# Performance work log

Hardware: AMD Instinct MI355X
Metric: run time of the kernel (lower is better)

Reference implementation:

```python
import jax, jax.numpy as jnp
import numpy as np

EMBED_DIM = 768
NUM_HEADS = 12
HEAD_DIM = EMBED_DIM // NUM_HEADS


def setup_inputs() -> dict:
    key = jax.random.key(0)
    k1, k2, k3 = jax.random.split(key, 3)
    B, T = 128, 128
    x = jax.random.normal(k1, (B, T, EMBED_DIM), dtype=jnp.float32)
    # weights stored as [in, out] so forward is x @ W (equivalent to torch Linear, bias=False)
    w_qkv = jax.random.normal(k2, (EMBED_DIM, 3 * EMBED_DIM), dtype=jnp.float32) * (EMBED_DIM ** -0.5)
    w_proj = jax.random.normal(k3, (EMBED_DIM, EMBED_DIM), dtype=jnp.float32) * (EMBED_DIM ** -0.5)
    return {"x": x, "w_qkv": w_qkv, "w_proj": w_proj}


def reference(x, w_qkv, w_proj):
    B, T, C = x.shape
    # fused QKV projection -> (3, B, H, T, D)
    qkv = (x @ w_qkv).reshape(B, T, 3, NUM_HEADS, HEAD_DIM)
    q, k, v = jnp.transpose(qkv, (2, 0, 3, 1, 4))
    # scaled dot-product scores (B, H, T, T)
    att = jnp.einsum('bhqd,bhkd->bhqk', q, k) * (HEAD_DIM ** -0.5)
    causal = jnp.tril(jnp.ones((T, T), dtype=bool))
    att = jnp.where(causal, att, -jnp.inf)
    # float32 softmax then cast back (matches att.float().softmax().to(x.dtype))
    att = jax.nn.softmax(att.astype(jnp.float32), axis=-1).astype(x.dtype)
    # dropout is identity in eval/reference mode
    out = jnp.einsum('bhqk,bhkd->bhqd', att, v)          # (B, H, T, D)
    out = jnp.transpose(out, (0, 2, 1, 3)).reshape(B, T, C)
    return out @ w_proj
```

## Files before the change

kernel.cpp:

```cpp
#include <hip/hip_runtime.h>

typedef __bf16 bf16_t;
typedef bf16_t bf16x8 __attribute__((ext_vector_type(8)));
typedef bf16_t bf16x4 __attribute__((ext_vector_type(4)));
typedef float f32x4 __attribute__((ext_vector_type(4)));

__device__ __forceinline__ f32x4 mfma16(bf16x8 a, bf16x8 b, f32x4 c) {
  return __builtin_amdgcn_mfma_f32_16x16x32_bf16(a, b, c, 0, 0, 0);
}

__device__ __forceinline__ void gload16(const bf16_t* g, bf16_t* l) {
  __builtin_amdgcn_global_load_lds(
      (const __attribute__((address_space(1))) void*)g,
      (__attribute__((address_space(3))) void*)l, 16, 0, 0);
}

__global__ void convert_kernel(const float* __restrict__ in, bf16_t* __restrict__ out, int n4) {
  int i = blockIdx.x * blockDim.x + threadIdx.x;
  if (i < n4) {
    float4 v = ((const float4*)in)[i];
    bf16x4 o;
    o[0] = (bf16_t)v.x; o[1] = (bf16_t)v.y; o[2] = (bf16_t)v.z; o[3] = (bf16_t)v.w;
    *(bf16x4*)&out[(size_t)i * 4] = o;
  }
}

__global__ void transpose_conv_kernel(const float* __restrict__ in, bf16_t* __restrict__ out,
                                      int K, int N) {
  __shared__ bf16_t tile[32][33];
  const int n0 = blockIdx.x * 32, k0 = blockIdx.y * 32;
  const int tx = threadIdx.x & 31, ty = threadIdx.x >> 5;
#pragma unroll
  for (int ph = 0; ph < 4; ++ph) {
    int k = ty + ph * 8;
    tile[k][tx] = (bf16_t)in[(size_t)(k0 + k) * N + n0 + tx];
  }
  __syncthreads();
#pragma unroll
  for (int ph = 0; ph < 4; ++ph) {
    int n = ty + ph * 8;
    out[(size_t)(n0 + n) * K + k0 + tx] = tile[tx][n];
  }
}

template <bool F32OUT>
__global__ __launch_bounds__(256, 2) void gemm_kernel(
    const bf16_t* __restrict__ A, const bf16_t* __restrict__ Bt,
    void* __restrict__ Cout, int M, int N, int K) {
  __shared__ bf16_t As[2][128 * 64];
  __shared__ bf16_t Bs[2][128 * 64];
  const int tid = threadIdx.x;
  const int lane = tid & 63;
  const int w = tid >> 6;
  const int wm = w >> 1, wn = w & 1;
  const int lr = lane & 15, kg = lane >> 4;
  const int bm = blockIdx.y, bn = blockIdx.x;
  const bf16_t* Ab = A + (size_t)bm * 128 * K;
  const bf16_t* Bb = Bt + (size_t)bn * 128 * K;

  f32x4 acc[4][4];
#pragma unroll
  for (int i = 0; i < 4; ++i)
#pragma unroll
    for (int j = 0; j < 4; ++j) acc[i][j] = (f32x4){0.f, 0.f, 0.f, 0.f};

  const int NKT = K >> 6;
  const int sr = tid >> 3;
  const int sslot = tid & 7;

  auto stage = [&](int buf, int kt) {
    const int k0 = kt << 6;
#pragma unroll
    for (int it = 0; it < 4; ++it) {
      int r = it * 32 + sr;
      int kofs = (sslot ^ (r & 7)) << 3;
      int lidx = (it * 256 + tid) << 3;
      gload16(Ab + (size_t)r * K + (k0 + kofs), &As[buf][lidx]);
      gload16(Bb + (size_t)r * K + (k0 + kofs), &Bs[buf][lidx]);
    }
  };

  stage(0, 0);
  __syncthreads();

  for (int kt = 0; kt < NKT; ++kt) {
    const int buf = kt & 1;
    if (kt + 1 < NKT) stage(buf ^ 1, kt + 1);
#pragma unroll
    for (int kk = 0; kk < 2; ++kk) {
      const int slot = ((kk << 2) + kg) ^ (lr & 7);
      bf16x8 af[4], bfv[4];
#pragma unroll
      for (int mt = 0; mt < 4; ++mt) {
        int r = wm * 64 + mt * 16 + lr;
        af[mt] = *(const bf16x8*)&As[buf][(r << 6) + (slot << 3)];
      }
#pragma unroll
      for (int nt = 0; nt < 4; ++nt) {
        int r = wn * 64 + nt * 16 + lr;
        bfv[nt] = *(const bf16x8*)&Bs[buf][(r << 6) + (slot << 3)];
      }
#pragma unroll
      for (int mt = 0; mt < 4; ++mt)
#pragma unroll
        for (int nt = 0; nt < 4; ++nt)
          acc[mt][nt] = mfma16(af[mt], bfv[nt], acc[mt][nt]);
    }
    __syncthreads();
  }

  const int row0 = bm * 128 + wm * 64 + kg * 4;
  const int col0 = bn * 128 + wn * 64 + lr;
#pragma unroll
  for (int mt = 0; mt < 4; ++mt)
#pragma unroll
    for (int nt = 0; nt < 4; ++nt)
#pragma unroll
      for (int rr = 0; rr < 4; ++rr) {
        size_t idx = (size_t)(row0 + mt * 16 + rr) * N + (col0 + nt * 16);
        if constexpr (F32OUT)
          ((float*)Cout)[idx] = acc[mt][nt][rr];
        else
          ((bf16_t*)Cout)[idx] = (bf16_t)acc[mt][nt][rr];
      }
}

#define ATT_H 12
__global__ __launch_bounds__(256, 2) void attn_kernel(const bf16_t* __restrict__ qkv,
                                                      bf16_t* __restrict__ obuf) {
  __shared__ bf16_t Ks[128 * 72];
  __shared__ bf16_t Vt[64 * 136];
  __shared__ bf16_t Ps[128 * 136];
  const int tid = threadIdx.x, lane = tid & 63, w = tid >> 6;
  const int lr = lane & 15, kg = lane >> 4;
  const int bh = blockIdx.x;
  const int b = bh / ATT_H, h = bh % ATT_H;
  const size_t base = (size_t)b * 128 * 2304;
  const int hoff = h * 64;

#pragma unroll
  for (int it = 0; it < 4; ++it) {
    int idx = it * 256 + tid;
    int r = idx >> 3, slot = idx & 7;
    bf16x8 v = *(const bf16x8*)&qkv[base + (size_t)r * 2304 + 768 + hoff + slot * 8];
    *(bf16x8*)&Ks[r * 72 + slot * 8] = v;
  }
#pragma unroll 4
  for (int it = 0; it < 32; ++it) {
    int idx = it * 256 + tid;
    int t = idx >> 6, d = idx & 63;
    Vt[d * 136 + t] = qkv[base + (size_t)t * 2304 + 1536 + hoff + d];
  }
  const int qrow0 = w * 32;
  bf16x8 qf[2][2];
#pragma unroll
  for (int mt = 0; mt < 2; ++mt)
#pragma unroll
    for (int kk = 0; kk < 2; ++kk)
      qf[mt][kk] = *(const bf16x8*)&qkv[base + (size_t)(qrow0 + mt * 16 + lr) * 2304 + hoff +
                                        kk * 32 + kg * 8];
  __syncthreads();

  const int NT = 2 * w + 2;
  f32x4 acc[2][8];
#pragma unroll
  for (int mt = 0; mt < 2; ++mt)
#pragma unroll
    for (int nt = 0; nt < 8; ++nt) acc[mt][nt] = (f32x4){0.f, 0.f, 0.f, 0.f};

#pragma unroll
  for (int nt = 0; nt < 8; ++nt) {
    if (nt < NT) {
#pragma unroll
      for (int kk = 0; kk < 2; ++kk) {
        bf16x8 kf = *(const bf16x8*)&Ks[(nt * 16 + lr) * 72 + kk * 32 + kg * 8];
        acc[0][nt] = mfma16(qf[0][kk], kf, acc[0][nt]);
        acc[1][nt] = mfma16(qf[1][kk], kf, acc[1][nt]);
      }
    }
  }

#pragma unroll
  for (int mt = 0; mt < 2; ++mt) {
#pragma unroll
    for (int rr = 0; rr < 4; ++rr) {
      const int row = qrow0 + mt * 16 + kg * 4 + rr;
      float m = -1e30f;
#pragma unroll
      for (int nt = 0; nt < 8; ++nt) {
        if (nt < NT) {
          int col = nt * 16 + lr;
          float s = acc[mt][nt][rr] * 0.125f;
          s = (col <= row) ? s : -1e30f;
          acc[mt][nt][rr] = s;
          m = fmaxf(m, s);
        }
      }
      m = fmaxf(m, __shfl_xor(m, 1));
      m = fmaxf(m, __shfl_xor(m, 2));
      m = fmaxf(m, __shfl_xor(m, 4));
      m = fmaxf(m, __shfl_xor(m, 8));
      float ssum = 0.f;
#pragma unroll
      for (int nt = 0; nt < 8; ++nt) {
        if (nt < NT) {
          float p = __builtin_amdgcn_exp2f((acc[mt][nt][rr] - m) * 1.44269504f);
          acc[mt][nt][rr] = p;
          ssum += p;
        }
      }
      ssum += __shfl_xor(ssum, 1);
      ssum += __shfl_xor(ssum, 2);
      ssum += __shfl_xor(ssum, 4);
      ssum += __shfl_xor(ssum, 8);
      float inv = 1.0f / ssum;
#pragma unroll
      for (int nt = 0; nt < 8; ++nt) {
        if (nt < NT) Ps[row * 136 + nt * 16 + lr] = (bf16_t)(acc[mt][nt][rr] * inv);
      }
    }
  }

  f32x4 oacc[2][4];
#pragma unroll
  for (int mt = 0; mt < 2; ++mt)
#pragma unroll
    for (int dt = 0; dt < 4; ++dt) oacc[mt][dt] = (f32x4){0.f, 0.f, 0.f, 0.f};

  const int KS = w + 1;
#pragma unroll
  for (int ks = 0; ks < 4; ++ks) {
    if (ks < KS) {
      bf16x8 pa0 = *(const bf16x8*)&Ps[(qrow0 + lr) * 136 + ks * 32 + kg * 8];
      bf16x8 pa1 = *(const bf16x8*)&Ps[(qrow0 + 16 + lr) * 136 + ks * 32 + kg * 8];
#pragma unroll
      for (int dt = 0; dt < 4; ++dt) {
        bf16x8 vb = *(const bf16x8*)&Vt[(dt * 16 + lr) * 136 + ks * 32 + kg * 8];
        oacc[0][dt] = mfma16(pa0, vb, oacc[0][dt]);
        oacc[1][dt] = mfma16(pa1, vb, oacc[1][dt]);
      }
    }
  }

#pragma unroll
  for (int mt = 0; mt < 2; ++mt)
#pragma unroll
    for (int dt = 0; dt < 4; ++dt)
#pragma unroll
      for (int rr = 0; rr < 4; ++rr) {
        int t = qrow0 + mt * 16 + kg * 4 + rr;
        obuf[((size_t)b * 128 + t) * 768 + hoff + dt * 16 + lr] = (bf16_t)oacc[mt][dt][rr];
      }
}

extern "C" void kernel_launch(void* const* d_in, const int* in_sizes, int n_in,
                              void* d_out, int out_size, void* d_ws, size_t ws_size,
                              hipStream_t stream) {
  const float* x = (const float*)d_in[0];
  const float* w_qkv = (const float*)d_in[1];
  const float* w_proj = (const float*)d_in[2];
  float* out = (float*)d_out;
  char* ws = (char*)d_ws;

  bf16_t* xb     = (bf16_t*)(ws);
  bf16_t* wqkvt  = (bf16_t*)(ws + 25165824);
  bf16_t* wprojt = (bf16_t*)(ws + 28704768);
  bf16_t* qkv    = (bf16_t*)(ws + 29884416);
  bf16_t* obuf   = (bf16_t*)(ws + 105381888);

  convert_kernel<<<dim3(12288), dim3(256), 0, stream>>>(x, xb, 3145728);
  transpose_conv_kernel<<<dim3(72, 24), dim3(256), 0, stream>>>(w_qkv, wqkvt, 768, 2304);
  transpose_conv_kernel<<<dim3(24, 24), dim3(256), 0, stream>>>(w_proj, wprojt, 768, 768);
  gemm_kernel<false><<<dim3(18, 128), dim3(256), 0, stream>>>(xb, wqkvt, (void*)qkv, 16384, 2304, 768);
  attn_kernel<<<dim3(1536), dim3(256), 0, stream>>>(qkv, obuf);
  gemm_kernel<true><<<dim3(6, 128), dim3(256), 0, stream>>>(obuf, wprojt, (void*)out, 16384, 768, 768);
}
```

Baseline: 172.2 us.

## Replace GEMM with 256x256 8-wave pipelined kernel and XCD-aware block swizzle

Both projection GEMMs now use a new 512-thread kernel computing 256x256 output tiles, where each wave owns a 128x64 sub-tile. Global-to-LDS loads for later k-tiles are interleaved between MFMA quads under explicit vmcnt waits and barriers, and MFMA priority is raised with setprio. The 1D grid is remapped so consecutive tiles land on the same XCD for better L2 reuse. This aims to hide load latency and cut LDS traffic per FLOP. In exchange it uses 128KB of LDS per block, adds many barriers, and leaves fewer blocks for the small output projection (192 blocks).

```diff
diff --git a/kernel.cpp b/kernel.cpp
--- a/kernel.cpp
+++ b/kernel.cpp
@@ -14,6 +14,14 @@
       (const __attribute__((address_space(1))) void*)g,
       (__attribute__((address_space(3))) void*)l, 16, 0, 0);
 }
+
+#define BARRIER()                      \
+  do {                                 \
+    asm volatile("" ::: "memory");     \
+    __builtin_amdgcn_s_barrier();      \
+    asm volatile("" ::: "memory");     \
+  } while (0)
+#define VMCNT(n) asm volatile("s_waitcnt vmcnt(" #n ")" ::: "memory")
 
 __global__ void convert_kernel(const float* __restrict__ in, bf16_t* __restrict__ out, int n4) {
   int i = blockIdx.x * blockDim.x + threadIdx.x;
@@ -44,75 +52,148 @@
 }
 
 template <bool F32OUT>
-__global__ __launch_bounds__(256, 2) void gemm_kernel(
+__global__ __launch_bounds__(512, 2) void gemm8_kernel(
     const bf16_t* __restrict__ A, const bf16_t* __restrict__ Bt,
-    void* __restrict__ Cout, int M, int N, int K) {
-  __shared__ bf16_t As[2][128 * 64];
-  __shared__ bf16_t Bs[2][128 * 64];
+    void* __restrict__ Cout, int M, int N, int K, int nbn) {
+  __shared__ bf16_t As[2][256 * 64];
+  __shared__ bf16_t Bs[2][256 * 64];
   const int tid = threadIdx.x;
   const int lane = tid & 63;
   const int w = tid >> 6;
-  const int wm = w >> 1, wn = w & 1;
+  const int wm = w >> 2, wn = w & 3;
   const int lr = lane & 15, kg = lane >> 4;
-  const int bm = blockIdx.y, bn = blockIdx.x;
-  const bf16_t* Ab = A + (size_t)bm * 128 * K;
-  const bf16_t* Bb = Bt + (size_t)bn * 128 * K;
-
-  f32x4 acc[4][4];
-#pragma unroll
-  for (int i = 0; i < 4; ++i)
+
+  const int nwg = gridDim.x;
+  const int cpx = nwg >> 3;
+  const int bid = blockIdx.x;
+  const int sid = (bid & 7) * cpx + (bid >> 3);
+  const int bm = sid / nbn, bn = sid % nbn;
+
+  const bf16_t* Ab = A + (size_t)bm * 256 * K;
+  const bf16_t* Bb = Bt + (size_t)bn * 256 * K;
+
+  f32x4 acc[8][4];
+#pragma unroll
+  for (int i = 0; i < 8; ++i)
 #pragma unroll
     for (int j = 0; j < 4; ++j) acc[i][j] = (f32x4){0.f, 0.f, 0.f, 0.f};
 
   const int NKT = K >> 6;
-  const int sr = tid >> 3;
-  const int sslot = tid & 7;
-
-  auto stage = [&](int buf, int kt) {
-    const int k0 = kt << 6;
-#pragma unroll
-    for (int it = 0; it < 4; ++it) {
-      int r = it * 32 + sr;
-      int kofs = (sslot ^ (r & 7)) << 3;
-      int lidx = (it * 256 + tid) << 3;
-      gload16(Ab + (size_t)r * K + (k0 + kofs), &As[buf][lidx]);
-      gload16(Bb + (size_t)r * K + (k0 + kofs), &Bs[buf][lidx]);
-    }
-  };
-
-  stage(0, 0);
-  __syncthreads();
-
-  for (int kt = 0; kt < NKT; ++kt) {
-    const int buf = kt & 1;
-    if (kt + 1 < NKT) stage(buf ^ 1, kt + 1);
-#pragma unroll
-    for (int kk = 0; kk < 2; ++kk) {
-      const int slot = ((kk << 2) + kg) ^ (lr & 7);
-      bf16x8 af[4], bfv[4];
-#pragma unroll
-      for (int mt = 0; mt < 4; ++mt) {
-        int r = wm * 64 + mt * 16 + lr;
-        af[mt] = *(const bf16x8*)&As[buf][(r << 6) + (slot << 3)];
-      }
-#pragma unroll
-      for (int nt = 0; nt < 4; ++nt) {
-        int r = wn * 64 + nt * 16 + lr;
-        bfv[nt] = *(const bf16x8*)&Bs[buf][(r << 6) + (slot << 3)];
-      }
-#pragma unroll
-      for (int mt = 0; mt < 4; ++mt)
-#pragma unroll
-        for (int nt = 0; nt < 4; ++nt)
-          acc[mt][nt] = mfma16(af[mt], bfv[nt], acc[mt][nt]);
-    }
-    __syncthreads();
-  }
-
-  const int row0 = bm * 128 + wm * 64 + kg * 4;
-  const int col0 = bn * 128 + wn * 64 + lr;
-#pragma unroll
-  for (int mt = 0; mt < 4; ++mt)
+  const int NIT = NKT >> 1;
+
+  auto stageAbs = [&](int tau, int part) {
+    const int h = part & 1;
+    const bf16_t* Pb = (part < 2) ? Ab : Bb;
+    bf16_t* Ls = (part < 2) ? &As[tau & 1][0] : &Bs[tau & 1][0];
+    const int k0 = tau << 6;
+#pragma unroll
+    for (int j = 0; j < 2; ++j) {
+      int idx = j * 512 + tid;
+      int rl = idx >> 3, p = idx & 7;
+      gload16(Pb + (size_t)(h * 128 + rl) * K + (k0 + ((p ^ (rl & 7)) << 3)),
+              Ls + h * 8192 + idx * 8);
+    }
+  };
+  auto stageHT = [&](int g) {
+    if (g < 0) return;
+    int tau = 2 + (g >> 2);
+    if (tau >= NKT) return;
+    stageAbs(tau, g & 3);
+  };
+
+  auto readA = [&](int slot, int mh, bf16x8 aF[4][2]) {
+#pragma unroll
+    for (int mq = 0; mq < 4; ++mq) {
+      int r = wm * 128 + mh * 64 + mq * 16 + lr;
+#pragma unroll
+      for (int kk = 0; kk < 2; ++kk) {
+        int c = ((kk << 2) + kg) ^ (lr & 7);
+        aF[mq][kk] = *(const bf16x8*)&As[slot][r * 64 + c * 8];
+      }
+    }
+  };
+  auto readB = [&](int slot, int nh, bf16x8 bF[2][2]) {
+#pragma unroll
+    for (int nq = 0; nq < 2; ++nq) {
+      int r = wn * 64 + (nh * 2 + nq) * 16 + lr;
+#pragma unroll
+      for (int kk = 0; kk < 2; ++kk) {
+        int c = ((kk << 2) + kg) ^ (lr & 7);
+        bF[nq][kk] = *(const bf16x8*)&Bs[slot][r * 64 + c * 8];
+      }
+    }
+  };
+  auto quad = [&](int mh, int nh, bf16x8 aF[4][2], bf16x8 bF[2][2]) {
+    __builtin_amdgcn_s_setprio(1);
+#pragma unroll
+    for (int mq = 0; mq < 4; ++mq)
+#pragma unroll
+      for (int nq = 0; nq < 2; ++nq)
+#pragma unroll
+        for (int kk = 0; kk < 2; ++kk)
+          acc[mh * 4 + mq][nh * 2 + nq] =
+              mfma16(aF[mq][kk], bF[nq][kk], acc[mh * 4 + mq][nh * 2 + nq]);
+    __builtin_amdgcn_s_setprio(0);
+  };
+
+#pragma unroll
+  for (int part = 0; part < 4; ++part) stageAbs(0, part);
+#pragma unroll
+  for (int part = 0; part < 4; ++part) stageAbs(1, part);
+  VMCNT(8);
+  BARRIER();
+
+  bf16x8 aF0[4][2], aF1[4][2], bF[2][2];
+  for (int it = 0; it < NIT; ++it) {
+    const int g0 = it * 8;
+    readA(0, 0, aF0);
+    readB(0, 0, bF);
+    stageHT(g0 - 2);
+    BARRIER();
+    quad(0, 0, aF0, bF);
+    BARRIER();
+    readA(0, 1, aF1);
+    stageHT(g0 - 1);
+    BARRIER();
+    quad(1, 0, aF1, bF);
+    BARRIER();
+    readB(0, 1, bF);
+    stageHT(g0 + 0);
+    BARRIER();
+    quad(1, 1, aF1, bF);
+    BARRIER();
+    stageHT(g0 + 1);
+    VMCNT(4);
+    BARRIER();
+    quad(0, 1, aF0, bF);
+    BARRIER();
+    readA(1, 0, aF0);
+    readB(1, 0, bF);
+    stageHT(g0 + 2);
+    BARRIER();
+    quad(0, 0, aF0, bF);
+    BARRIER();
+    readA(1, 1, aF1);
+    stageHT(g0 + 3);
+    BARRIER();
+    quad(1, 0, aF1, bF);
+    BARRIER();
+    readB(1, 1, bF);
+    stageHT(g0 + 4);
+    BARRIER();
+    quad(1, 1, aF1, bF);
+    BARRIER();
+    stageHT(g0 + 5);
+    VMCNT(4);
+    BARRIER();
+    quad(0, 1, aF0, bF);
+    BARRIER();
+  }
+
+  const int row0 = bm * 256 + wm * 128 + kg * 4;
+  const int col0 = bn * 256 + wn * 64 + lr;
+#pragma unroll
+  for (int mt = 0; mt < 8; ++mt)
 #pragma unroll
     for (int nt = 0; nt < 4; ++nt)
 #pragma unroll
@@ -271,7 +352,7 @@
   convert_kernel<<<dim3(12288), dim3(256), 0, stream>>>(x, xb, 3145728);
   transpose_conv_kernel<<<dim3(72, 24), dim3(256), 0, stream>>>(w_qkv, wqkvt, 768, 2304);
   transpose_conv_kernel<<<dim3(24, 24), dim3(256), 0, stream>>>(w_proj, wprojt, 768, 768);
-  gemm_kernel<false><<<dim3(18, 128), dim3(256), 0, stream>>>(xb, wqkvt, (void*)qkv, 16384, 2304, 768);
+  gemm8_kernel<false><<<dim3(576), dim3(512), 0, stream>>>(xb, wqkvt, (void*)qkv, 16384, 2304, 768, 9);
   attn_kernel<<<dim3(1536), dim3(256), 0, stream>>>(qkv, obuf);
-  gemm_kernel<true><<<dim3(6, 128), dim3(256), 0, stream>>>(obuf, wprojt, (void*)out, 16384, 768, 768);
-}
+  gemm8_kernel<true><<<dim3(192), dim3(512), 0, stream>>>(obuf, wprojt, (void*)out, 16384, 768, 768, 3);
+}
```

New measurement: 168.9 us. Within noise of the previous version (-1.9%).

## Make GEMMs persistent with cross-tile prefetch and fuse prep kernels

Applied to the files above, without the earlier changes.

Merges the x conversion and both weight transposes into one prep launch. Replaces the tiled GEMM with a persistent kernel where each block walks a contiguous range of output tiles and prefetches the next tile's first K-slice during the current tile's last iteration. It uses an XCD-aware block remap, BN=64 tiles for the projection GEMM, and raises the launch-bounds occupancy hint to 3. The aim is to cut launch overhead and tail/wave-quantization effects. The cost is extra index logic and more pressure on registers and LDS per CU.

```diff
diff --git a/kernel.cpp b/kernel.cpp
--- a/kernel.cpp
+++ b/kernel.cpp
@@ -15,114 +15,147 @@
       (__attribute__((address_space(3))) void*)l, 16, 0, 0);
 }
 
-__global__ void convert_kernel(const float* __restrict__ in, bf16_t* __restrict__ out, int n4) {
-  int i = blockIdx.x * blockDim.x + threadIdx.x;
-  if (i < n4) {
-    float4 v = ((const float4*)in)[i];
+__global__ void prep_kernel(const float* __restrict__ x, const float* __restrict__ wq,
+                            const float* __restrict__ wp, bf16_t* __restrict__ xb,
+                            bf16_t* __restrict__ wqt, bf16_t* __restrict__ wpt) {
+  __shared__ bf16_t tile[32][33];
+  const int bid = blockIdx.x;
+  if (bid < 12288) {
+    int i = bid * 256 + threadIdx.x;
+    float4 v = ((const float4*)x)[i];
     bf16x4 o;
     o[0] = (bf16_t)v.x; o[1] = (bf16_t)v.y; o[2] = (bf16_t)v.z; o[3] = (bf16_t)v.w;
-    *(bf16x4*)&out[(size_t)i * 4] = o;
-  }
-}
-
-__global__ void transpose_conv_kernel(const float* __restrict__ in, bf16_t* __restrict__ out,
-                                      int K, int N) {
-  __shared__ bf16_t tile[32][33];
-  const int n0 = blockIdx.x * 32, k0 = blockIdx.y * 32;
-  const int tx = threadIdx.x & 31, ty = threadIdx.x >> 5;
+    *(bf16x4*)&xb[(size_t)i * 4] = o;
+    return;
+  }
+  const int t = bid - 12288;
+  const int ty = t / 96, txb = t % 96;
+  const float* in;
+  bf16_t* out;
+  int N, n0;
+  if (txb < 72) { in = wq; out = wqt; N = 2304; n0 = txb * 32; }
+  else          { in = wp; out = wpt; N = 768;  n0 = (txb - 72) * 32; }
+  const int k0 = ty * 32;
+  const int tx = threadIdx.x & 31, tyy = threadIdx.x >> 5;
 #pragma unroll
   for (int ph = 0; ph < 4; ++ph) {
-    int k = ty + ph * 8;
+    int k = tyy + ph * 8;
     tile[k][tx] = (bf16_t)in[(size_t)(k0 + k) * N + n0 + tx];
   }
   __syncthreads();
 #pragma unroll
   for (int ph = 0; ph < 4; ++ph) {
-    int n = ty + ph * 8;
-    out[(size_t)(n0 + n) * K + k0 + tx] = tile[tx][n];
-  }
-}
-
-template <bool F32OUT>
-__global__ __launch_bounds__(256, 2) void gemm_kernel(
+    int n = tyy + ph * 8;
+    out[(size_t)(n0 + n) * 768 + k0 + tx] = tile[tx][n];
+  }
+}
+
+template <int BN, bool F32OUT>
+__global__ __launch_bounds__(256, 3) void gemm_persist(
     const bf16_t* __restrict__ A, const bf16_t* __restrict__ Bt,
-    void* __restrict__ Cout, int M, int N, int K) {
+    void* __restrict__ Cout, int N, int K, int nbn, int q, int r) {
+  constexpr int NQ = BN / 32;
   __shared__ bf16_t As[2][128 * 64];
-  __shared__ bf16_t Bs[2][128 * 64];
+  __shared__ bf16_t Bs[2][BN * 64];
   const int tid = threadIdx.x;
   const int lane = tid & 63;
   const int w = tid >> 6;
   const int wm = w >> 1, wn = w & 1;
   const int lr = lane & 15, kg = lane >> 4;
-  const int bm = blockIdx.y, bn = blockIdx.x;
-  const bf16_t* Ab = A + (size_t)bm * 128 * K;
-  const bf16_t* Bb = Bt + (size_t)bn * 128 * K;
-
-  f32x4 acc[4][4];
-#pragma unroll
-  for (int i = 0; i < 4; ++i)
-#pragma unroll
-    for (int j = 0; j < 4; ++j) acc[i][j] = (f32x4){0.f, 0.f, 0.f, 0.f};
+
+  const int G = gridDim.x;
+  const int bid = blockIdx.x;
+  const int lb = (bid & 7) * (G >> 3) + (bid >> 3);
+  int nj, start;
+  if (lb < r) { nj = q + 1; start = lb * (q + 1); }
+  else        { nj = q;     start = r * (q + 1) + (lb - r) * q; }
 
   const int NKT = K >> 6;
-  const int sr = tid >> 3;
-  const int sslot = tid & 7;
-
-  auto stage = [&](int buf, int kt) {
-    const int k0 = kt << 6;
+  const int sr = tid >> 3, sslot = tid & 7;
+
+  auto stage = [&](int buf, const bf16_t* Aj, const bf16_t* Bj, int k0) {
 #pragma unroll
     for (int it = 0; it < 4; ++it) {
-      int r = it * 32 + sr;
-      int kofs = (sslot ^ (r & 7)) << 3;
-      int lidx = (it * 256 + tid) << 3;
-      gload16(Ab + (size_t)r * K + (k0 + kofs), &As[buf][lidx]);
-      gload16(Bb + (size_t)r * K + (k0 + kofs), &Bs[buf][lidx]);
+      int rr = it * 32 + sr;
+      gload16(Aj + (size_t)rr * K + (k0 + ((sslot ^ (rr & 7)) << 3)),
+              &As[buf][(it * 256 + tid) * 8]);
+    }
+#pragma unroll
+    for (int it = 0; it < NQ; ++it) {
+      int rr = it * 32 + sr;
+      gload16(Bj + (size_t)rr * K + (k0 + ((sslot ^ (rr & 7)) << 3)),
+              &Bs[buf][(it * 256 + tid) * 8]);
     }
   };
 
-  stage(0, 0);
+  int job = start;
+  int bm = job / nbn, bn = job % nbn;
+  const bf16_t* Aj = A + (size_t)bm * 128 * K;
+  const bf16_t* Bj = Bt + (size_t)bn * BN * K;
+  stage(0, Aj, Bj, 0);
   __syncthreads();
-
-  for (int kt = 0; kt < NKT; ++kt) {
-    const int buf = kt & 1;
-    if (kt + 1 < NKT) stage(buf ^ 1, kt + 1);
-#pragma unroll
-    for (int kk = 0; kk < 2; ++kk) {
-      const int slot = ((kk << 2) + kg) ^ (lr & 7);
-      bf16x8 af[4], bfv[4];
-#pragma unroll
-      for (int mt = 0; mt < 4; ++mt) {
-        int r = wm * 64 + mt * 16 + lr;
-        af[mt] = *(const bf16x8*)&As[buf][(r << 6) + (slot << 3)];
-      }
-#pragma unroll
-      for (int nt = 0; nt < 4; ++nt) {
-        int r = wn * 64 + nt * 16 + lr;
-        bfv[nt] = *(const bf16x8*)&Bs[buf][(r << 6) + (slot << 3)];
-      }
-#pragma unroll
-      for (int mt = 0; mt < 4; ++mt)
-#pragma unroll
-        for (int nt = 0; nt < 4; ++nt)
-          acc[mt][nt] = mfma16(af[mt], bfv[nt], acc[mt][nt]);
-    }
-    __syncthreads();
-  }
-
-  const int row0 = bm * 128 + wm * 64 + kg * 4;
-  const int col0 = bn * 128 + wn * 64 + lr;
-#pragma unroll
-  for (int mt = 0; mt < 4; ++mt)
-#pragma unroll
-    for (int nt = 0; nt < 4; ++nt)
-#pragma unroll
-      for (int rr = 0; rr < 4; ++rr) {
-        size_t idx = (size_t)(row0 + mt * 16 + rr) * N + (col0 + nt * 16);
-        if constexpr (F32OUT)
-          ((float*)Cout)[idx] = acc[mt][nt][rr];
-        else
-          ((bf16_t*)Cout)[idx] = (bf16_t)acc[mt][nt][rr];
-      }
+  int buf = 0;
+
+  for (int j = 0; j < nj; ++j) {
+    f32x4 acc[4][NQ];
+#pragma unroll
+    for (int i = 0; i < 4; ++i)
+#pragma unroll
+      for (int n = 0; n < NQ; ++n) acc[i][n] = (f32x4){0.f, 0.f, 0.f, 0.f};
+
+    int nbm = 0, nbnx = 0;
+    const bf16_t *nAj = nullptr, *nBj = nullptr;
+    if (j + 1 < nj) {
+      int njob = job + 1;
+      nbm = njob / nbn; nbnx = njob % nbn;
+      nAj = A + (size_t)nbm * 128 * K;
+      nBj = Bt + (size_t)nbnx * BN * K;
+    }
+
+    for (int kt = 0; kt < NKT; ++kt) {
+      if (kt + 1 < NKT)      stage(buf ^ 1, Aj, Bj, (kt + 1) << 6);
+      else if (j + 1 < nj)   stage(buf ^ 1, nAj, nBj, 0);
+#pragma unroll
+      for (int kk = 0; kk < 2; ++kk) {
+        const int slot = ((kk << 2) + kg) ^ (lr & 7);
+        bf16x8 af[4], bfv[NQ];
+#pragma unroll
+        for (int mq = 0; mq < 4; ++mq) {
+          int rr = wm * 64 + mq * 16 + lr;
+          af[mq] = *(const bf16x8*)&As[buf][(rr << 6) + (slot << 3)];
+        }
+#pragma unroll
+        for (int nq = 0; nq < NQ; ++nq) {
+          int rr = wn * (BN / 2) + nq * 16 + lr;
+          bfv[nq] = *(const bf16x8*)&Bs[buf][(rr << 6) + (slot << 3)];
+        }
+#pragma unroll
+        for (int mq = 0; mq < 4; ++mq)
+#pragma unroll
+          for (int nq = 0; nq < NQ; ++nq)
+            acc[mq][nq] = mfma16(af[mq], bfv[nq], acc[mq][nq]);
+      }
+      __syncthreads();
+      buf ^= 1;
+    }
+
+    const int row0 = bm * 128 + wm * 64 + kg * 4;
+    const int col0 = bn * BN + wn * (BN / 2) + lr;
+#pragma unroll
+    for (int mq = 0; mq < 4; ++mq)
+#pragma unroll
+      for (int nq = 0; nq < NQ; ++nq)
+#pragma unroll
+        for (int rr = 0; rr < 4; ++rr) {
+          size_t idx = (size_t)(row0 + mq * 16 + rr) * N + (col0 + nq * 16);
+          if constexpr (F32OUT)
+            ((float*)Cout)[idx] = acc[mq][nq][rr];
+          else
+            ((bf16_t*)Cout)[idx] = (bf16_t)acc[mq][nq][rr];
+        }
+
+    job++; bm = nbm; bn = nbnx; Aj = nAj; Bj = nBj;
+  }
 }
 
 #define ATT_H 12
@@ -268,10 +301,10 @@
   bf16_t* qkv    = (bf16_t*)(ws + 29884416);
   bf16_t* obuf   = (bf16_t*)(ws + 105381888);
 
-  convert_kernel<<<dim3(12288), dim3(256), 0, stream>>>(x, xb, 3145728);
-  transpose_conv_kernel<<<dim3(72, 24), dim3(256), 0, stream>>>(w_qkv, wqkvt, 768, 2304);
-  transpose_conv_kernel<<<dim3(24, 24), dim3(256), 0, stream>>>(w_proj, wprojt, 768, 768);
-  gemm_kernel<false><<<dim3(18, 128), dim3(256), 0, stream>>>(xb, wqkvt, (void*)qkv, 16384, 2304, 768);
+  prep_kernel<<<dim3(12288 + 2304), dim3(256), 0, stream>>>(x, w_qkv, w_proj, xb, wqkvt, wprojt);
+  gemm_persist<128, false><<<dim3(512), dim3(256), 0, stream>>>(
+      xb, wqkvt, (void*)qkv, 2304, 768, 18, 4, 256);
   attn_kernel<<<dim3(1536), dim3(256), 0, stream>>>(qkv, obuf);
-  gemm_kernel<true><<<dim3(6, 128), dim3(256), 0, stream>>>(obuf, wprojt, (void*)out, 16384, 768, 768);
-}
+  gemm_persist<64, true><<<dim3(768), dim3(256), 0, stream>>>(
+      obuf, wprojt, (void*)out, 768, 768, 12, 2, 0);
+}
```

Measured after the change: 157.9 us. 8.3% less time.
